# Kernel tuning notes

Measured on AMD Instinct MI355X. Metric: run time of the kernel, lower is better.

## Reference

```python
import jax, jax.numpy as jnp
import numpy as np

B, H, S, Dh = 8, 16, 1028, 64
G = 32
L2 = (2 * G - 1) ** 2  # 3969 relative-position entries
HID = 32
R_VAL = 4  # register-token cutoff


def setup_inputs() -> dict:
    key = jax.random.key(0)
    ks = jax.random.split(key, 7)
    return {
        "q": jax.random.normal(ks[0], (B, H, S, Dh), jnp.float32),
        "k": jax.random.normal(ks[1], (B, H, S, Dh), jnp.float32),
        "v": jax.random.normal(ks[2], (B, H, S, Dh), jnp.float32),
        # normalized log-spaced relative coords in [-1, 1], Swin-v2 style
        "rel_table": jax.random.uniform(ks[3], (L2, 2), jnp.float32, -1.0, 1.0),
        "W1": jax.random.normal(ks[4], (2, HID), jnp.float32) * 0.1,
        "b1": jnp.zeros((HID,), jnp.float32),
        "W2": jax.random.normal(ks[5], (HID, H), jnp.float32) * 0.02,
        "idx_table": jax.random.randint(ks[6], (S, S), 0, L2, jnp.int32),
        "R": R_VAL,
    }


def reference(q, k, v, rel_table, W1, b1, W2, idx_table, R):
    # CPB MLP: Linear(2->hid) + exact GELU + Linear(hid->H, no bias)
    bt = jax.nn.gelu(rel_table @ W1 + b1, approximate=False) @ W2  # [L2, H]
    # gather per-(q,kv) bias, move head axis front -> [H, S, S]
    bias = jnp.transpose(bt[idx_table], (2, 0, 1))
    pos = jnp.arange(S) >= R
    has_bias = pos[:, None] & pos[None, :]  # [S, S]
    scale = Dh ** -0.5
    scores = jnp.einsum('bhqd,bhkd->bhqk', q, k) * scale  # [B,H,S,S]
    scores = scores + jnp.where(has_bias, bias, 0.0)[None]
    p = jax.nn.softmax(scores, axis=-1)
    return jnp.einsum('bhqk,bhkd->bhqd', p, v)
```

## Files before the change

kernel.cpp:

```cpp
#include <hip/hip_runtime.h>
#include <hip/hip_bf16.h>

#define S_LEN 1028
#define DH 64
#define NHEAD 16
#define NBATCH 8
#define L2N 3969
#define HIDN 32
#define KVB 64
#define NKT 17
#define NQT 17
#define TILE_E 4096
#define LOG2E 1.4426950408889634f
#define NKV_TILES (NKT * NBATCH * NHEAD)

typedef __bf16 bf16x8 __attribute__((ext_vector_type(8)));
typedef __bf16 bf16x4 __attribute__((ext_vector_type(4)));
typedef float f32x4 __attribute__((ext_vector_type(4)));

__device__ __forceinline__ bf16x8 cvt_bf16x8(float4 a, float4 b) {
  bf16x8 r;
  r[0] = (__bf16)a.x; r[1] = (__bf16)a.y; r[2] = (__bf16)a.z; r[3] = (__bf16)a.w;
  r[4] = (__bf16)b.x; r[5] = (__bf16)b.y; r[6] = (__bf16)b.z; r[7] = (__bf16)b.w;
  return r;
}

__device__ __forceinline__ f32x4 mfma16(bf16x8 a, bf16x8 b, f32x4 c) {
  return __builtin_amdgcn_mfma_f32_16x16x32_bf16(a, b, c, 0, 0, 0);
}

__device__ __forceinline__ float exp2_fast(float x) {
#if __has_builtin(__builtin_amdgcn_exp2f)
  return __builtin_amdgcn_exp2f(x);
#else
  return __expf(x * 0.6931471805599453f);
#endif
}

#define GLD16(gsrc, ldst)                                                     \
  __builtin_amdgcn_global_load_lds(                                           \
      (const __attribute__((address_space(1))) void*)(gsrc),                  \
      (__attribute__((address_space(3))) void*)(ldst), 16, 0, 0)

__global__ void cpb_table_lh(const float* __restrict__ rel,
                             const float* __restrict__ W1,
                             const float* __restrict__ b1,
                             const float* __restrict__ W2,
                             float* __restrict__ bt,
                             __bf16* __restrict__ bt16) {
  int i = blockIdx.x * blockDim.x + threadIdx.x;
  if (i >= L2N) return;
  float x = rel[2 * i], y = rel[2 * i + 1];
  float acc[NHEAD];
#pragma unroll
  for (int h = 0; h < NHEAD; ++h) acc[h] = 0.f;
#pragma unroll
  for (int j = 0; j < HIDN; ++j) {
    float t = fmaf(x, W1[j], fmaf(y, W1[HIDN + j], b1[j]));
    float g = 0.5f * t * (1.f + erff(t * 0.70710678118654752f));
#pragma unroll
    for (int h = 0; h < NHEAD; ++h) acc[h] = fmaf(g, W2[j * NHEAD + h], acc[h]);
  }
#pragma unroll
  for (int h = 0; h < NHEAD; ++h) {
    bt[(size_t)i * NHEAD + h] = acc[h];
    bt16[(size_t)i * NHEAD + h] = (__bf16)(acc[h] * LOG2E);
  }
}

__global__ __launch_bounds__(256) void prep_fused2(
    const int* __restrict__ idx, const __bf16* __restrict__ bt16,
    const int* __restrict__ Rp, const float* __restrict__ kg,
    const float* __restrict__ vg, __bf16* __restrict__ bias,
    __bf16* __restrict__ Kb, __bf16* __restrict__ Vb) {
  const int tid = threadIdx.x;
  const int bid = blockIdx.x;
  __shared__ __align__(16) char smem[64 * 68 * 4];

  int kvid = -1, qrow = -1;
  if (bid < 3084) {
    const int grp = bid / 3, rem = bid - 3 * grp;
    if (rem == 0) qrow = grp;
    else kvid = 2 * grp + (rem - 1);
  } else {
    kvid = 2056 + (bid - 3084);
  }

  if (qrow >= 0) {
    __bf16(*strip)[520] = (__bf16(*)[520])smem;
    const int R = Rp[0];
    const bool qok = (qrow >= R);
    const __bf16* bsrc = bt16;
    bf16x8 z8;
#pragma unroll
    for (int j = 0; j < 8; ++j) z8[j] = (__bf16)0.f;

    for (int k0 = 0; k0 < 1024; k0 += 512) {
      const int ka = k0 + tid, kb2 = k0 + 256 + tid;
      const int la = idx[(size_t)qrow * S_LEN + ka];
      const int lb = idx[(size_t)qrow * S_LEN + kb2];
      bf16x8 va0 = *(const bf16x8*)(bsrc + (size_t)la * 16);
      bf16x8 va1 = *(const bf16x8*)(bsrc + (size_t)la * 16 + 8);
      bf16x8 vb0 = *(const bf16x8*)(bsrc + (size_t)lb * 16);
      bf16x8 vb1 = *(const bf16x8*)(bsrc + (size_t)lb * 16 + 8);
      const bool ona = qok && (ka >= R);
      const bool onb = qok && (kb2 >= R);
      if (!ona) { va0 = z8; va1 = z8; }
      if (!onb) { vb0 = z8; vb1 = z8; }
#pragma unroll
      for (int h = 0; h < 8; ++h) {
        strip[h][tid] = va0[h];
        strip[h][256 + tid] = vb0[h];
        strip[8 + h][tid] = va1[h];
        strip[8 + h][256 + tid] = vb1[h];
      }
      __syncthreads();
      {
        const int h = tid >> 4, seg = tid & 15;
        __bf16* dst = bias + (size_t)h * S_LEN * S_LEN + (size_t)qrow * S_LEN +
                      k0 + seg * 32;
#pragma unroll
        for (int j = 0; j < 4; ++j) {
          bf16x8 w = *(bf16x8*)&strip[h][seg * 32 + j * 8];
          *(bf16x4*)(dst + j * 8) = *(bf16x4*)&w;
          *(bf16x4*)(dst + j * 8 + 4) = *((bf16x4*)&w + 1);
        }
      }
      __syncthreads();
    }
    if (tid < 64) {
      const int kt = tid & 3, h = tid >> 2;
      const int k = 1024 + kt;
      const int l = idx[(size_t)qrow * S_LEN + k];
      const bool on = qok && (k >= R);
      bias[(size_t)h * S_LEN * S_LEN + (size_t)qrow * S_LEN + k] =
          on ? bt16[(size_t)l * 16 + h] : (__bf16)0.f;
    }
  } else {
    if (kvid >= NKV_TILES) return;
    const int it = kvid % NKT, bh = kvid / NKT;
    const int kb = it * KVB;
    const float* kp = kg + (size_t)bh * S_LEN * DH;
    const float* vp = vg + (size_t)bh * S_LEN * DH;
    __bf16* kout = Kb + ((size_t)bh * NKT + it) * TILE_E;
    __bf16* vout = Vb + ((size_t)bh * NKT + it) * TILE_E;

    for (int i = tid; i < 512; i += 256) {
      const int rho = i >> 3, gx = i & 7;
      const int e = ((rho & 15) << 2) | (rho >> 4);
      const int key = kb + e;
      const int gsrc = gx ^ (rho & 7);
      float4 a = {0.f, 0.f, 0.f, 0.f}, b = {0.f, 0.f, 0.f, 0.f};
      if (key < S_LEN) {
        a = *(const float4*)(kp + (size_t)key * DH + gsrc * 8);
        b = *(const float4*)(kp + (size_t)key * DH + gsrc * 8 + 4);
      }
      *(bf16x8*)(kout + (size_t)rho * 64 + gx * 8) = cvt_bf16x8(a, b);
    }

    float(*vt)[68] = (float(*)[68])smem;
    for (int i = tid; i < 1024; i += 256) {
      const int row = i >> 4, c4 = i & 15;
      const int key = kb + row;
      float4 a = {0.f, 0.f, 0.f, 0.f};
      if (key < S_LEN) a = *(const float4*)(vp + (size_t)key * DH + c4 * 4);
      *(float4*)&vt[row][c4 * 4] = a;
    }
    __syncthreads();
    for (int i = tid; i < 512; i += 256) {
      const int d = i >> 3, gx = i & 7;
      const int kg8 = (gx ^ (d & 7)) * 8;
      bf16x8 o;
#pragma unroll
      for (int j = 0; j < 8; ++j) o[j] = (__bf16)vt[kg8 + j][d];
      *(bf16x8*)(vout + (size_t)d * 64 + gx * 8) = o;
    }
  }
}

#define TILE_STEP(ITC, MASKED) do {                                           \
    const int buf_ = (ITC) & 1;                                               \
    const int kk_ = (ITC) * KVB + 4 * m;                                      \
    bf16x4 bias4_[4];                                                         \
    _Pragma("unroll")                                                         \
    for (int r = 0; r < 4; ++r) {                                             \
      bf16x4 z_; z_[0] = (__bf16)0.f; z_[1] = (__bf16)0.f;                    \
      z_[2] = (__bf16)0.f; z_[3] = (__bf16)0.f;                               \
      bias4_[r] = (!(MASKED) || kk_ < S_LEN)                                  \
                      ? *(const bf16x4*)(brow[r] + kk_) : z_;                 \
    }                                                                         \
    __builtin_amdgcn_s_barrier();                                             \
    {                                                                         \
      const int nit_ = ((ITC) + 1 < NKT) ? (ITC) + 1 : 0;                     \
      const __bf16* gk_ = KbT + (size_t)nit_ * TILE_E + wave * 1024 + lo16;   \
      const __bf16* gv_ = VbT + (size_t)nit_ * TILE_E + wave * 1024 + lo16;   \
      __bf16* lk_ = &Kt[buf_ ^ 1][0][0] + wave * 1024;                        \
      __bf16* lv_ = &Vt[buf_ ^ 1][0][0] + wave * 1024;                        \
      GLD16(gk_, lk_); GLD16(gk_ + 512, lk_ + 512);                           \
      GLD16(gv_, lv_); GLD16(gv_ + 512, lv_ + 512);                           \
    }                                                                         \
    asm volatile("s_waitcnt vmcnt(8)" ::: "memory");                          \
    __builtin_amdgcn_s_barrier();                                             \
    __builtin_amdgcn_sched_barrier(0);                                        \
    f32x4 sc_[4];                                                             \
    _Pragma("unroll")                                                         \
    for (int c = 0; c < 4; ++c) {                                             \
      f32x4 a_;                                                               \
      _Pragma("unroll")                                                       \
      for (int r = 0; r < 4; ++r) a_[r] = (float)bias4_[r][c];                \
      _Pragma("unroll")                                                       \
      for (int dc = 0; dc < 2; ++dc) {                                        \
        bf16x8 kf_ = *(bf16x8*)&Kt[buf_][c * 16 + m][(dc * 32 + g * 8) ^ sw_m]; \
        a_ = mfma16(qf[dc], kf_, a_);                                         \
      }                                                                       \
      sc_[c] = a_;                                                            \
    }                                                                         \
    _Pragma("unroll")                                                         \
    for (int r = 0; r < 4; ++r) {                                             \
      float p0_ = exp2_fast(sc_[0][r]);                                       \
      float p1_ = exp2_fast(sc_[1][r]);                                       \
      float p2_ = exp2_fast(sc_[2][r]);                                       \
      float p3_ = exp2_fast(sc_[3][r]);                                       \
      if (MASKED) {                                                           \
        const float kvf_ = (kk_ < S_LEN) ? 1.f : 0.f;                         \
        lsum[r] += kvf_ * ((p0_ + p1_) + (p2_ + p3_));                        \
      } else {                                                                \
        lsum[r] += (p0_ + p1_) + (p2_ + p3_);                                 \
      }                                                                       \
      bf16x4 pb_;                                                             \
      pb_[0] = (__bf16)p0_; pb_[1] = (__bf16)p1_;                             \
      pb_[2] = (__bf16)p2_; pb_[3] = (__bf16)p3_;                             \
      const int row_ = g * 4 + r;                                             \
      *(bf16x4*)&Pl[wave][row_][(4 * m) ^ ((row_ & 7) << 3)] = pb_;           \
    }                                                                         \
    _Pragma("unroll")                                                         \
    for (int kc = 0; kc < 2; ++kc) {                                          \
      bf16x8 pf_ = *(bf16x8*)&Pl[wave][m][(kc * 32 + g * 8) ^ sw_m];          \
      _Pragma("unroll")                                                       \
      for (int t = 0; t < 4; ++t) {                                           \
        bf16x8 vf_ = *(bf16x8*)&Vt[buf_][t * 16 + m][(kc * 32 + g * 8) ^ sw_m]; \
        acc_o[t] = mfma16(pf_, vf_, acc_o[t]);                                \
      }                                                                       \
    }                                                                         \
  } while (0)

__global__ __launch_bounds__(256, 4) void flex_attn_v4x(
    const float* __restrict__ qg, const __bf16* __restrict__ Kb,
    const __bf16* __restrict__ Vb, const __bf16* __restrict__ biasG,
    float* __restrict__ out) {
  const int h = blockIdx.x;
  const int y = blockIdx.y;
  const int qt = y % NQT;
  const int b = y / NQT;
  const int bh = b * NHEAD + h;
  const int tid = threadIdx.x;
  const int wave = tid >> 6, lane = tid & 63;
  const int g = lane >> 4, m = lane & 15;

  __shared__ __align__(16) __bf16 Kt[2][KVB][64];
  __shared__ __align__(16) __bf16 Vt[2][DH][64];
  __shared__ __align__(16) __bf16 Pl[4][16][64];

  const __bf16* KbT = Kb + (size_t)bh * NKT * TILE_E;
  const __bf16* VbT = Vb + (size_t)bh * NKT * TILE_E;
  const __bf16* bp = biasG + (size_t)h * S_LEN * S_LEN;
  const float* qp = qg + (size_t)bh * S_LEN * DH;

  const int qrow = qt * 64 + wave * 16 + m;
  const float qs = 0.125f * LOG2E;
  bf16x8 qf[2];
#pragma unroll
  for (int dc = 0; dc < 2; ++dc) {
    float4 a = {0.f, 0.f, 0.f, 0.f}, bb = {0.f, 0.f, 0.f, 0.f};
    if (qrow < S_LEN) {
      a = *(const float4*)(qp + (size_t)qrow * DH + dc * 32 + g * 8);
      bb = *(const float4*)(qp + (size_t)qrow * DH + dc * 32 + g * 8 + 4);
    }
    a.x *= qs; a.y *= qs; a.z *= qs; a.w *= qs;
    bb.x *= qs; bb.y *= qs; bb.z *= qs; bb.w *= qs;
    qf[dc] = cvt_bf16x8(a, bb);
  }

  const int qb4 = qt * 64 + wave * 16 + g * 4;
  const __bf16* brow[4];
#pragma unroll
  for (int r = 0; r < 4; ++r) {
    int qq = qb4 + r; if (qq > S_LEN - 1) qq = S_LEN - 1;
    brow[r] = bp + (size_t)qq * S_LEN;
  }

  f32x4 acc_o[4];
#pragma unroll
  for (int t = 0; t < 4; ++t) acc_o[t] = (f32x4){0.f, 0.f, 0.f, 0.f};
  float lsum[4] = {0.f, 0.f, 0.f, 0.f};

  const int sw_m = (m & 7) << 3;
  const int lo16 = lane * 8;

  {
    const __bf16* gk = KbT + wave * 1024 + lo16;
    const __bf16* gv = VbT + wave * 1024 + lo16;
    __bf16* lk = &Kt[0][0][0] + wave * 1024;
    __bf16* lv = &Vt[0][0][0] + wave * 1024;
    GLD16(gk, lk); GLD16(gk + 512, lk + 512);
    GLD16(gv, lv); GLD16(gv + 512, lv + 512);
  }

#pragma unroll 2
  for (int it = 0; it < 16; ++it) {
    TILE_STEP(it, false);
  }
  TILE_STEP(16, true);

#pragma unroll
  for (int r = 0; r < 4; ++r) {
    float s = lsum[r];
    s += __shfl_xor(s, 1);
    s += __shfl_xor(s, 2);
    s += __shfl_xor(s, 4);
    s += __shfl_xor(s, 8);
    const int qq = qb4 + r;
    if (qq >= S_LEN) continue;
    const float inv = 1.f / s;
    float* op = out + (((size_t)bh) * S_LEN + qq) * DH;
#pragma unroll
    for (int t = 0; t < 4; ++t) op[t * 16 + m] = acc_o[t][r] * inv;
  }
}

__global__ __launch_bounds__(256) void bias_expand2(const int* __restrict__ idx,
                                                    const float* __restrict__ bt,
                                                    const int* __restrict__ Rp,
                                                    __bf16* __restrict__ bias) {
  const int qrow = blockIdx.x;
  const int R = Rp[0];
  const bool qok = (qrow >= R);
  const int tid = threadIdx.x;
  __shared__ __align__(16) __bf16 strip[NHEAD][264];
  for (int k0 = 0; k0 < 1024; k0 += 256) {
    const int k = k0 + tid;
    const int l = idx[(size_t)qrow * S_LEN + k];
    const bool on = qok && (k >= R);
    const float4* btv = (const float4*)bt + (size_t)l * 4;
    float va[16];
    *(float4*)&va[0] = btv[0];
    *(float4*)&va[4] = btv[1];
    *(float4*)&va[8] = btv[2];
    *(float4*)&va[12] = btv[3];
#pragma unroll
    for (int h = 0; h < NHEAD; ++h)
      strip[h][tid] = on ? (__bf16)(va[h] * LOG2E) : (__bf16)0.f;
    __syncthreads();
    {
      const int h = tid >> 4, kg2 = tid & 15;
      bf16x8 w0 = *(bf16x8*)&strip[h][kg2 * 16];
      bf16x8 w1 = *(bf16x8*)&strip[h][kg2 * 16 + 8];
      __bf16* dst = bias + (size_t)h * S_LEN * S_LEN + (size_t)qrow * S_LEN + k0 + kg2 * 16;
      *(bf16x8*)dst = w0;
      *(bf16x8*)(dst + 8) = w1;
    }
    __syncthreads();
  }
  if (tid < 64) {
    const int kt = tid & 3, h = tid >> 2;
    const int k = 1024 + kt;
    const int l = idx[(size_t)qrow * S_LEN + k];
    const bool on = qok && (k >= R);
    const float v = bt[(size_t)l * NHEAD + h];
    bias[(size_t)h * S_LEN * S_LEN + (size_t)qrow * S_LEN + k] =
        on ? (__bf16)(v * LOG2E) : (__bf16)0.f;
  }
}

__global__ __launch_bounds__(256, 4) void flex_attn_fast(
    const float* __restrict__ qg, const float* __restrict__ kg,
    const float* __restrict__ vg, const __bf16* __restrict__ biasG,
    float* __restrict__ out) {
  const int b = blockIdx.z, h = blockIdx.y, qt = blockIdx.x;
  const int tid = threadIdx.x;
  const int wave = tid >> 6, lane = tid & 63;
  const int g = lane >> 4, m = lane & 15;

  __shared__ __align__(16) __bf16 Kt[KVB][72];
  __shared__ __align__(16) __bf16 Vt[DH][72];
  __shared__ __align__(16) __bf16 Pl[4][16][72];

  const size_t base = ((size_t)(b * NHEAD + h)) * S_LEN * DH;
  const float* qp = qg + base;
  const float* kp = kg + base;
  const float* vp = vg + base;
  const __bf16* bp = biasG + (size_t)h * S_LEN * S_LEN;

  const int qrow = qt * 64 + wave * 16 + m;
  const float qs = 0.125f * LOG2E;
  bf16x8 qf[2];
#pragma unroll
  for (int dc = 0; dc < 2; ++dc) {
    float4 a = {0.f, 0.f, 0.f, 0.f}, bb = {0.f, 0.f, 0.f, 0.f};
    if (qrow < S_LEN) {
      a = *(const float4*)(qp + (size_t)qrow * DH + dc * 32 + g * 8);
      bb = *(const float4*)(qp + (size_t)qrow * DH + dc * 32 + g * 8 + 4);
    }
    a.x *= qs; a.y *= qs; a.z *= qs; a.w *= qs;
    bb.x *= qs; bb.y *= qs; bb.z *= qs; bb.w *= qs;
    qf[dc] = cvt_bf16x8(a, bb);
  }

  f32x4 acc_o[4];
#pragma unroll
  for (int t = 0; t < 4; ++t) acc_o[t] = (f32x4){0.f, 0.f, 0.f, 0.f};
  float mrow[4], lrow[4];
#pragma unroll
  for (int r = 0; r < 4; ++r) { mrow[r] = -1e30f; lrow[r] = 0.f; }

  const int qb4 = qt * 64 + wave * 16 + g * 4;
  const int eK = wave * 16 + (lane >> 2);
  const int rowK = ((eK & 3) << 4) | (eK >> 2);
  const int colK = (lane & 3) * 16;

  for (int it = 0; it < NKT; ++it) {
    const int kb = it * KVB;
    __syncthreads();
    {
      const int krow = kb + eK;
      float4 a0 = {0,0,0,0}, a1 = {0,0,0,0}, a2 = {0,0,0,0}, a3 = {0,0,0,0};
      if (krow < S_LEN) {
        const float* src = kp + (size_t)krow * DH + colK;
        a0 = *(const float4*)(src);
        a1 = *(const float4*)(src + 4);
        a2 = *(const float4*)(src + 8);
        a3 = *(const float4*)(src + 12);
      }
      *(bf16x8*)&Kt[rowK][colK] = cvt_bf16x8(a0, a1);
      *(bf16x8*)&Kt[rowK][colK + 8] = cvt_bf16x8(a2, a3);
    }
    {
      bf16x8 p0, p1;
#pragma unroll
      for (int t = 0; t < 8; ++t) {
        const int kr = kb + wave * 16 + t;
        p0[t] = (kr < S_LEN) ? (__bf16)vp[(size_t)kr * DH + lane] : (__bf16)0.f;
      }
#pragma unroll
      for (int t = 0; t < 8; ++t) {
        const int kr = kb + wave * 16 + 8 + t;
        p1[t] = (kr < S_LEN) ? (__bf16)vp[(size_t)kr * DH + lane] : (__bf16)0.f;
      }
      *(bf16x8*)&Vt[lane][wave * 16] = p0;
      *(bf16x8*)&Vt[lane][wave * 16 + 8] = p1;
    }

    const int kk = kb + 4 * m;
    const bool kvalid = (kk < S_LEN);
    bf16x4 bias4[4];
#pragma unroll
    for (int r = 0; r < 4; ++r) {
      const int qq = (qb4 + r < S_LEN) ? qb4 + r : S_LEN - 1;
      bf16x4 z; z[0] = (__bf16)0.f; z[1] = (__bf16)0.f; z[2] = (__bf16)0.f; z[3] = (__bf16)0.f;
      bias4[r] = kvalid ? *(const bf16x4*)(bp + (size_t)qq * S_LEN + kk) : z;
    }

    __syncthreads();

    f32x4 sc[4];
#pragma unroll
    for (int c = 0; c < 4; ++c) {
      f32x4 a = (f32x4){0.f, 0.f, 0.f, 0.f};
#pragma unroll
      for (int dc = 0; dc < 2; ++dc) {
        bf16x8 kf = *(bf16x8*)&Kt[c * 16 + m][dc * 32 + g * 8];
        a = mfma16(qf[dc], kf, a);
      }
      sc[c] = a;
    }

#pragma unroll
    for (int r = 0; r < 4; ++r) {
      float s[4];
#pragma unroll
      for (int c = 0; c < 4; ++c)
        s[c] = kvalid ? sc[c][r] + (float)bias4[r][c] : -1e30f;
      float mx = fmaxf(fmaxf(s[0], s[1]), fmaxf(s[2], s[3]));
      mx = fmaxf(mx, __shfl_xor(mx, 1));
      mx = fmaxf(mx, __shfl_xor(mx, 2));
      mx = fmaxf(mx, __shfl_xor(mx, 4));
      mx = fmaxf(mx, __shfl_xor(mx, 8));
      const float mnew = fmaxf(mrow[r], mx);
      const float alpha = exp2_fast(mrow[r] - mnew);
      float p0 = exp2_fast(s[0] - mnew), p1 = exp2_fast(s[1] - mnew);
      float p2 = exp2_fast(s[2] - mnew), p3 = exp2_fast(s[3] - mnew);
      float sum = (p0 + p1) + (p2 + p3);
      sum += __shfl_xor(sum, 1);
      sum += __shfl_xor(sum, 2);
      sum += __shfl_xor(sum, 4);
      sum += __shfl_xor(sum, 8);
      lrow[r] = lrow[r] * alpha + sum;
      mrow[r] = mnew;
      bf16x4 pb;
      pb[0] = (__bf16)p0; pb[1] = (__bf16)p1; pb[2] = (__bf16)p2; pb[3] = (__bf16)p3;
      *(bf16x4*)&Pl[wave][g * 4 + r][4 * m] = pb;
#pragma unroll
      for (int t = 0; t < 4; ++t) acc_o[t][r] *= alpha;
    }

#pragma unroll
    for (int kc = 0; kc < 2; ++kc) {
      bf16x8 pf = *(bf16x8*)&Pl[wave][m][kc * 32 + g * 8];
#pragma unroll
      for (int t = 0; t < 4; ++t) {
        bf16x8 vf = *(bf16x8*)&Vt[t * 16 + m][kc * 32 + g * 8];
        acc_o[t] = mfma16(pf, vf, acc_o[t]);
      }
    }
  }

#pragma unroll
  for (int r = 0; r < 4; ++r) {
    const int qq = qb4 + r;
    if (qq >= S_LEN) continue;
    const float inv = 1.f / lrow[r];
    float* op = out + (((size_t)(b * NHEAD + h)) * S_LEN + qq) * DH;
#pragma unroll
    for (int t = 0; t < 4; ++t) op[t * 16 + m] = acc_o[t][r] * inv;
  }
}

extern "C" void kernel_launch(void* const* d_in, const int* in_sizes, int n_in,
                              void* d_out, int out_size, void* d_ws, size_t ws_size,
                              hipStream_t stream) {
  const float* q = (const float*)d_in[0];
  const float* k = (const float*)d_in[1];
  const float* v = (const float*)d_in[2];
  const float* rel = (const float*)d_in[3];
  const float* W1 = (const float*)d_in[4];
  const float* b1 = (const float*)d_in[5];
  const float* W2 = (const float*)d_in[6];
  const int* idx = (const int*)d_in[7];
  const int* Rp = (const int*)d_in[8];
  float* out = (float*)d_out;

  const size_t bt_bytes = 1u << 18;
  const size_t bt16_bytes = 1u << 17;
  const size_t bias_bytes = (size_t)NHEAD * S_LEN * S_LEN * 2;
  const size_t kv_bytes = (size_t)NBATCH * NHEAD * NKT * TILE_E * 2;

  float* bt = (float*)d_ws;
  __bf16* bt16 = (__bf16*)((char*)d_ws + bt_bytes);
  __bf16* bias = (__bf16*)((char*)d_ws + bt_bytes + bt16_bytes);
  __bf16* Kb = (__bf16*)((char*)d_ws + bt_bytes + bt16_bytes + bias_bytes);
  __bf16* Vb = (__bf16*)((char*)d_ws + bt_bytes + bt16_bytes + bias_bytes + kv_bytes);

  if (ws_size >= bt_bytes + bt16_bytes + bias_bytes + 2 * kv_bytes) {
    cpb_table_lh<<<dim3((L2N + 255) / 256), dim3(256), 0, stream>>>(rel, W1, b1, W2, bt, bt16);
    prep_fused2<<<dim3(3204), dim3(256), 0, stream>>>(idx, bt16, Rp, k, v, bias, Kb, Vb);
    flex_attn_v4x<<<dim3(NHEAD, NQT * NBATCH, 1), dim3(256), 0, stream>>>(q, Kb, Vb, bias, out);
  } else {
    __bf16* bias_f = (__bf16*)((char*)d_ws + bt_bytes + bt16_bytes);
    cpb_table_lh<<<dim3((L2N + 255) / 256), dim3(256), 0, stream>>>(rel, W1, b1, W2, bt, bt16);
    bias_expand2<<<dim3(S_LEN), dim3(256), 0, stream>>>(idx, bt, Rp, bias_f);
    flex_attn_fast<<<dim3(NQT, NHEAD, NBATCH), dim3(256), 0, stream>>>(q, k, v, bias_f, out);
  }
}
```

Before: 252.7 us.

## Pad bias rows to aligned pitch, split bias prep blocks, add MFMA priority hints

The expanded bias tensor now uses a padded row pitch of 1040 elements, so each row starts 16-byte aligned and the prep kernel can write full 8-element vectors. Each bias row is now split across two blocks instead of one block looping over halves, which raises block count and removes a barrier round. The attention inner loop relaxes its scheduling barrier and raises wave priority around the MFMA sections to improve overlap. Costs are a somewhat larger bias workspace and possible scheduling side effects from the looser barrier mask.

```diff
diff --git a/kernel.cpp b/kernel.cpp
--- a/kernel.cpp
+++ b/kernel.cpp
@@ -13,6 +13,8 @@
 #define TILE_E 4096
 #define LOG2E 1.4426950408889634f
 #define NKV_TILES (NKT * NBATCH * NHEAD)
+#define SPITCH 1040
+#define SPLANE ((size_t)S_LEN * SPITCH)
 
 typedef __bf16 bf16x8 __attribute__((ext_vector_type(8)));
 typedef __bf16 bf16x4 __attribute__((ext_vector_type(4)));
@@ -68,7 +70,7 @@
   }
 }
 
-__global__ __launch_bounds__(256) void prep_fused2(
+__global__ __launch_bounds__(256) void prep_fused3(
     const int* __restrict__ idx, const __bf16* __restrict__ bt16,
     const int* __restrict__ Rp, const float* __restrict__ kg,
     const float* __restrict__ vg, __bf16* __restrict__ bias,
@@ -77,63 +79,56 @@
   const int bid = blockIdx.x;
   __shared__ __align__(16) char smem[64 * 68 * 4];
 
-  int kvid = -1, qrow = -1;
-  if (bid < 3084) {
-    const int grp = bid / 3, rem = bid - 3 * grp;
-    if (rem == 0) qrow = grp;
-    else kvid = 2 * grp + (rem - 1);
+  int kvid = -1, bias_id = -1;
+  if (bid < 4112) {
+    if ((bid & 1) == 0) bias_id = bid >> 1;
+    else kvid = bid >> 1;
   } else {
-    kvid = 2056 + (bid - 3084);
-  }
-
-  if (qrow >= 0) {
+    kvid = 2056 + (bid - 4112);
+  }
+
+  if (bias_id >= 0) {
+    const int qrow = bias_id >> 1, half = bias_id & 1;
+    const int base = half * 512;
     __bf16(*strip)[520] = (__bf16(*)[520])smem;
     const int R = Rp[0];
     const bool qok = (qrow >= R);
-    const __bf16* bsrc = bt16;
     bf16x8 z8;
 #pragma unroll
     for (int j = 0; j < 8; ++j) z8[j] = (__bf16)0.f;
 
-    for (int k0 = 0; k0 < 1024; k0 += 512) {
-      const int ka = k0 + tid, kb2 = k0 + 256 + tid;
-      const int la = idx[(size_t)qrow * S_LEN + ka];
-      const int lb = idx[(size_t)qrow * S_LEN + kb2];
-      bf16x8 va0 = *(const bf16x8*)(bsrc + (size_t)la * 16);
-      bf16x8 va1 = *(const bf16x8*)(bsrc + (size_t)la * 16 + 8);
-      bf16x8 vb0 = *(const bf16x8*)(bsrc + (size_t)lb * 16);
-      bf16x8 vb1 = *(const bf16x8*)(bsrc + (size_t)lb * 16 + 8);
-      const bool ona = qok && (ka >= R);
-      const bool onb = qok && (kb2 >= R);
-      if (!ona) { va0 = z8; va1 = z8; }
-      if (!onb) { vb0 = z8; vb1 = z8; }
-#pragma unroll
-      for (int h = 0; h < 8; ++h) {
-        strip[h][tid] = va0[h];
-        strip[h][256 + tid] = vb0[h];
-        strip[8 + h][tid] = va1[h];
-        strip[8 + h][256 + tid] = vb1[h];
-      }
-      __syncthreads();
-      {
-        const int h = tid >> 4, seg = tid & 15;
-        __bf16* dst = bias + (size_t)h * S_LEN * S_LEN + (size_t)qrow * S_LEN +
-                      k0 + seg * 32;
-#pragma unroll
-        for (int j = 0; j < 4; ++j) {
-          bf16x8 w = *(bf16x8*)&strip[h][seg * 32 + j * 8];
-          *(bf16x4*)(dst + j * 8) = *(bf16x4*)&w;
-          *(bf16x4*)(dst + j * 8 + 4) = *((bf16x4*)&w + 1);
-        }
-      }
-      __syncthreads();
-    }
-    if (tid < 64) {
+    const int ka = base + tid, kb2 = base + 256 + tid;
+    const int la = idx[(size_t)qrow * S_LEN + ka];
+    const int lb = idx[(size_t)qrow * S_LEN + kb2];
+    bf16x8 va0 = *(const bf16x8*)(bt16 + (size_t)la * 16);
+    bf16x8 va1 = *(const bf16x8*)(bt16 + (size_t)la * 16 + 8);
+    bf16x8 vb0 = *(const bf16x8*)(bt16 + (size_t)lb * 16);
+    bf16x8 vb1 = *(const bf16x8*)(bt16 + (size_t)lb * 16 + 8);
+    const bool ona = qok && (ka >= R);
+    const bool onb = qok && (kb2 >= R);
+    if (!ona) { va0 = z8; va1 = z8; }
+    if (!onb) { vb0 = z8; vb1 = z8; }
+#pragma unroll
+    for (int h = 0; h < 8; ++h) {
+      strip[h][tid] = va0[h];
+      strip[h][256 + tid] = vb0[h];
+      strip[8 + h][tid] = va1[h];
+      strip[8 + h][256 + tid] = vb1[h];
+    }
+    __syncthreads();
+    {
+      const int h = tid >> 4, seg = tid & 15;
+      __bf16* dst = bias + (size_t)h * SPLANE + (size_t)qrow * SPITCH + base + seg * 32;
+#pragma unroll
+      for (int j = 0; j < 4; ++j)
+        *(bf16x8*)(dst + j * 8) = *(bf16x8*)&strip[h][seg * 32 + j * 8];
+    }
+    if (half && tid < 64) {
       const int kt = tid & 3, h = tid >> 2;
       const int k = 1024 + kt;
       const int l = idx[(size_t)qrow * S_LEN + k];
       const bool on = qok && (k >= R);
-      bias[(size_t)h * S_LEN * S_LEN + (size_t)qrow * S_LEN + k] =
+      bias[(size_t)h * SPLANE + (size_t)qrow * SPITCH + k] =
           on ? bt16[(size_t)l * 16 + h] : (__bf16)0.f;
     }
   } else {
@@ -201,8 +196,9 @@
     }                                                                         \
     asm volatile("s_waitcnt vmcnt(8)" ::: "memory");                          \
     __builtin_amdgcn_s_barrier();                                             \
-    __builtin_amdgcn_sched_barrier(0);                                        \
+    __builtin_amdgcn_sched_barrier(0x7);   \
     f32x4 sc_[4];                                                             \
+    __builtin_amdgcn_s_setprio(1);                                            \
     _Pragma("unroll")                                                         \
     for (int c = 0; c < 4; ++c) {                                             \
       f32x4 a_;                                                               \
@@ -215,6 +211,7 @@
       }                                                                       \
       sc_[c] = a_;                                                            \
     }                                                                         \
+    __builtin_amdgcn_s_setprio(0);                                            \
     _Pragma("unroll")                                                         \
     for (int r = 0; r < 4; ++r) {                                             \
       float p0_ = exp2_fast(sc_[0][r]);                                       \
@@ -233,6 +230,7 @@
       const int row_ = g * 4 + r;                                             \
       *(bf16x4*)&Pl[wave][row_][(4 * m) ^ ((row_ & 7) << 3)] = pb_;           \
     }                                                                         \
+    __builtin_amdgcn_s_setprio(1);                                            \
     _Pragma("unroll")                                                         \
     for (int kc = 0; kc < 2; ++kc) {                                          \
       bf16x8 pf_ = *(bf16x8*)&Pl[wave][m][(kc * 32 + g * 8) ^ sw_m];          \
@@ -242,6 +240,7 @@
         acc_o[t] = mfma16(pf_, vf_, acc_o[t]);                                \
       }                                                                       \
     }                                                                         \
+    __builtin_amdgcn_s_setprio(0);                                            \
   } while (0)
 
 __global__ __launch_bounds__(256, 4) void flex_attn_v4x(
@@ -263,7 +262,7 @@
 
   const __bf16* KbT = Kb + (size_t)bh * NKT * TILE_E;
   const __bf16* VbT = Vb + (size_t)bh * NKT * TILE_E;
-  const __bf16* bp = biasG + (size_t)h * S_LEN * S_LEN;
+  const __bf16* bp = biasG + (size_t)h * SPLANE;
   const float* qp = qg + (size_t)bh * S_LEN * DH;
 
   const int qrow = qt * 64 + wave * 16 + m;
@@ -286,7 +285,7 @@
 #pragma unroll
   for (int r = 0; r < 4; ++r) {
     int qq = qb4 + r; if (qq > S_LEN - 1) qq = S_LEN - 1;
-    brow[r] = bp + (size_t)qq * S_LEN;
+    brow[r] = bp + (size_t)qq * SPITCH;
   }
 
   f32x4 acc_o[4];
@@ -541,7 +540,7 @@
 
   const size_t bt_bytes = 1u << 18;
   const size_t bt16_bytes = 1u << 17;
-  const size_t bias_bytes = (size_t)NHEAD * S_LEN * S_LEN * 2;
+  const size_t bias_bytes = (size_t)NHEAD * SPLANE * 2;
   const size_t kv_bytes = (size_t)NBATCH * NHEAD * NKT * TILE_E * 2;
 
   float* bt = (float*)d_ws;
@@ -552,7 +551,7 @@
 
   if (ws_size >= bt_bytes + bt16_bytes + bias_bytes + 2 * kv_bytes) {
     cpb_table_lh<<<dim3((L2N + 255) / 256), dim3(256), 0, stream>>>(rel, W1, b1, W2, bt, bt16);
-    prep_fused2<<<dim3(3204), dim3(256), 0, stream>>>(idx, bt16, Rp, k, v, bias, Kb, Vb);
+    prep_fused3<<<dim3(4232), dim3(256), 0, stream>>>(idx, bt16, Rp, k, v, bias, Kb, Vb);
     flex_attn_v4x<<<dim3(NHEAD, NQT * NBATCH, 1), dim3(256), 0, stream>>>(q, Kb, Vb, bias, out);
   } else {
     __bf16* bias_f = (__bf16*)((char*)d_ws + bt_bytes + bt16_bytes);
```

New measurement: 247.1 us. 1.02x faster.
